# Kernel optimization log

Hardware: AMD Instinct MI355X
Metric: run time of the kernel (lower is better)

The kernel has to match this reference:

```python
import jax, jax.numpy as jnp
import numpy as np

B, DIM, H, W = 8, 128, 64, 64
C, DI, N, R, K = DIM // 4, 2 * (DIM // 4), 16, 2, 4  # chunk dim, d_inner, d_state, dt_rank, n_dirs
L = H * W
EPS = 1e-5


def dwconv(x, w, b, dil):
    # x: [B,C,H,W]; w: [C,1,kh,kw] depthwise; torch padding='same' with dilation
    y = jax.lax.conv_general_dilated(
        x, w, window_strides=(1, 1), padding='SAME', rhs_dilation=(dil, dil),
        dimension_numbers=('NCHW', 'OIHW', 'NCHW'), feature_group_count=x.shape[1])
    return y + b[None, :, None, None]


def layernorm(x, w, b):
    mu = jnp.mean(x, -1, keepdims=True)
    var = jnp.var(x, -1, keepdims=True)
    return (x - mu) * jax.lax.rsqrt(var + EPS) * w + b


def axial_dw(x, mh_w, mh_b, mw_w, mw_b, c_w, c_b, dil):
    skip = x
    x = dwconv(x, mw_w, mw_b, dil)   # (1,7) kernel
    x = dwconv(x, mh_w, mh_b, dil)   # (7,1) kernel
    x = dwconv(x, c_w, c_b, dil)     # 3x3 kernel
    return x + skip


def ss2d(x, in_proj_w, conv_w, conv_b, x_proj_w, dt_proj_w, dt_proj_b,
         A_log, D, out_norm_w, out_norm_b, out_proj_w):
    # x: [B,H,W,C] channels-last (VMamba SS2D)
    b, h, w, _ = x.shape
    xz = jnp.einsum('bhwc,ec->bhwe', x, in_proj_w)          # [B,H,W,2*DI]
    xc, z = jnp.split(xz, 2, axis=-1)
    xc = xc.transpose(0, 3, 1, 2)                           # [B,DI,H,W]
    xc = jax.nn.silu(dwconv(xc, conv_w, conv_b, 1))
    l = h * w
    x_hw = xc.reshape(b, DI, l)
    x_wh = xc.transpose(0, 1, 3, 2).reshape(b, DI, l)
    xs = jnp.stack([x_hw, x_wh], 1)                         # [B,2,DI,L]
    xs = jnp.concatenate([xs, jnp.flip(xs, -1)], 1)         # [B,4,DI,L]
    x_dbl = jnp.einsum('bkdl,kcd->bkcl', xs, x_proj_w)      # c = R+2N
    dts, Bs, Cs = x_dbl[:, :, :R], x_dbl[:, :, R:R + N], x_dbl[:, :, R + N:]
    dts = jnp.einsum('bkrl,kdr->bkdl', dts, dt_proj_w)
    delta = jax.nn.softplus(dts + dt_proj_b[None, :, :, None])  # [B,4,DI,L]
    A = -jnp.exp(A_log)                                     # [4,DI,N]

    def step(hst, inp):
        u_t, dt_t, B_t, C_t = inp  # [B,4,DI],[B,4,DI],[B,4,N],[B,4,N]
        dA = jnp.exp(dt_t[..., None] * A)                   # [B,4,DI,N]
        hst = hst * dA + (dt_t * u_t)[..., None] * B_t[:, :, None, :]
        y = jnp.einsum('bkdn,bkn->bkd', hst, C_t)
        return hst, y

    u_l = jnp.moveaxis(xs, -1, 0)
    dt_l = jnp.moveaxis(delta, -1, 0)
    B_l = jnp.moveaxis(Bs, -1, 0)
    C_l = jnp.moveaxis(Cs, -1, 0)
    h0 = jnp.zeros((b, K, DI, N), xc.dtype)
    _, ys = jax.lax.scan(step, h0, (u_l, dt_l, B_l, C_l))   # [L,B,4,DI]
    out_y = jnp.moveaxis(ys, 0, -1) + D[None, :, :, None] * xs  # [B,4,DI,L]

    inv_y = jnp.flip(out_y[:, 2:4], -1)
    wh_y = out_y[:, 1].reshape(b, DI, w, h).transpose(0, 1, 3, 2).reshape(b, DI, l)
    invwh_y = inv_y[:, 1].reshape(b, DI, w, h).transpose(0, 1, 3, 2).reshape(b, DI, l)
    y = out_y[:, 0] + inv_y[:, 0] + wh_y + invwh_y          # [B,DI,L]
    y = y.transpose(0, 2, 1).reshape(b, h, w, DI)
    y = layernorm(y, out_norm_w, out_norm_b)
    y = y * jax.nn.silu(z)
    return jnp.einsum('bhwd,cd->bhwc', y, out_proj_w)


def setup_inputs() -> dict:
    key = jax.random.key(0)
    ks = iter(jax.random.split(key, 64))
    nrm = lambda s, sc=0.05: jax.random.normal(next(ks), s, jnp.float32) * sc
    inp = {'x': jax.random.normal(next(ks), (B, DIM, H, W), jnp.float32)}
    for i in (1, 2, 3):
        inp[f'dw{i}_mh_w'] = nrm((C, 1, 7, 1), 0.1); inp[f'dw{i}_mh_b'] = nrm((C,), 0.02)
        inp[f'dw{i}_mw_w'] = nrm((C, 1, 1, 7), 0.1); inp[f'dw{i}_mw_b'] = nrm((C,), 0.02)
        inp[f'dw{i}_c_w'] = nrm((C, 1, 3, 3), 0.1); inp[f'dw{i}_c_b'] = nrm((C,), 0.02)
    inp['ln_w'] = jnp.ones((C,)); inp['ln_b'] = jnp.zeros((C,))
    inp['in_proj_w'] = nrm((2 * DI, C))
    inp['conv_w'] = nrm((DI, 1, 3, 3), 0.1); inp['conv_b'] = nrm((DI,), 0.02)
    inp['x_proj_w'] = nrm((K, R + 2 * N, DI))
    inp['dt_proj_w'] = nrm((K, DI, R), 0.1)
    inp['dt_proj_b'] = nrm((K, DI), 0.02)
    inp['A_log'] = jax.random.uniform(next(ks), (K, DI, N), jnp.float32, 0.0, 2.0)
    inp['D'] = jnp.ones((K, DI), jnp.float32)
    inp['out_norm_w'] = jnp.ones((DI,)); inp['out_norm_b'] = jnp.zeros((DI,))
    inp['out_proj_w'] = nrm((C, DI))
    inp['bn_g'] = jnp.ones((DIM,)); inp['bn_b'] = jnp.zeros((DIM,))
    inp['bn_m'] = jnp.zeros((DIM,)); inp['bn_v'] = jnp.ones((DIM,))
    return inp


def reference(x, dw1_mh_w, dw1_mh_b, dw1_mw_w, dw1_mw_b, dw1_c_w, dw1_c_b,
              dw2_mh_w, dw2_mh_b, dw2_mw_w, dw2_mw_b, dw2_c_w, dw2_c_b,
              dw3_mh_w, dw3_mh_b, dw3_mw_w, dw3_mw_b, dw3_c_w, dw3_c_b,
              ln_w, ln_b, in_proj_w, conv_w, conv_b, x_proj_w, dt_proj_w, dt_proj_b,
              A_log, D, out_norm_w, out_norm_b, out_proj_w, bn_g, bn_b, bn_m, bn_v):
    def vss(xc):  # shared VSSBlock: [B,C,H,W] -> [B,C,H,W]
        t = xc.transpose(0, 2, 3, 1)
        t = t + ss2d(layernorm(t, ln_w, ln_b), in_proj_w, conv_w, conv_b, x_proj_w,
                     dt_proj_w, dt_proj_b, A_log, D, out_norm_w, out_norm_b, out_proj_w)
        return t.transpose(0, 3, 1, 2)

    x1, x2, x3, x4 = jnp.split(x, 4, axis=1)
    x1 = vss(axial_dw(x1, dw1_mh_w, dw1_mh_b, dw1_mw_w, dw1_mw_b, dw1_c_w, dw1_c_b, 1))
    x2 = vss(axial_dw(x2, dw2_mh_w, dw2_mh_b, dw2_mw_w, dw2_mw_b, dw2_c_w, dw2_c_b, 2))
    x3 = vss(axial_dw(x3, dw3_mh_w, dw3_mh_b, dw3_mw_w, dw3_mw_b, dw3_c_w, dw3_c_b, 3))
    xc = jnp.concatenate([x1, x2, x3, x4], axis=1)
    # BatchNorm2d in inference mode (running stats)
    y = (xc - bn_m[None, :, None, None]) * jax.lax.rsqrt(bn_v + EPS)[None, :, None, None]
    y = y * bn_g[None, :, None, None] + bn_b[None, :, None, None]
    return jax.nn.relu(y)
```

## Files before the change

### kernel.cpp

```cpp
#include <hip/hip_runtime.h>
#include <math.h>

#define LB __launch_bounds__(256)
#define LB512 __launch_bounds__(512)
#define LB64 __launch_bounds__(64)

#define LOG2E 1.44269504088896340736f
static __device__ __forceinline__ float silu_f(float x){ return x / (1.f + __expf(-x)); }
static __device__ __forceinline__ float softplus_f(float x){
    return (x > 20.f) ? x : __logf(1.f + __expf(x));
}

struct AxialArgs { const float* w[18]; };

__global__ LB void axial_kernel(const float* __restrict__ x, AxialArgs args,
    float* __restrict__ acc,
    const float* __restrict__ bn_g, const float* __restrict__ bn_b,
    const float* __restrict__ bn_m, const float* __restrict__ bn_v,
    float* __restrict__ out)
{
    __shared__ float s0[4096];
    __shared__ float s1[4096];
    if (blockIdx.x >= 768){
        const int gid = (blockIdx.x - 768)*256 + threadIdx.x;
        const int e = gid*4;
        const int l = e & 4095, bc = e >> 12;
        const int c = bc & 31, b = bc >> 5;
        const int ch = 96 + c;
        const size_t idx = ((size_t)b*128+ch)*4096 + l;
        float4 v = *(const float4*)&x[idx];
        const float sc = rsqrtf(bn_v[ch]+1e-5f)*bn_g[ch];
        const float mb = bn_m[ch], bbv = bn_b[ch];
        v.x = fmaxf((v.x-mb)*sc+bbv, 0.f);
        v.y = fmaxf((v.y-mb)*sc+bbv, 0.f);
        v.z = fmaxf((v.z-mb)*sc+bbv, 0.f);
        v.w = fmaxf((v.w-mb)*sc+bbv, 0.f);
        *(float4*)&out[idx] = v;
        return;
    }
    const int chunk = blockIdx.x >> 8;
    const int bc = blockIdx.x & 255;
    const int b = bc >> 5, c = bc & 31;
    const int dil = chunk + 1;
    const float* mh_w = args.w[chunk*6+0];
    const float* mh_b = args.w[chunk*6+1];
    const float* mw_w = args.w[chunk*6+2];
    const float* mw_b = args.w[chunk*6+3];
    const float* cw   = args.w[chunk*6+4];
    const float* cb   = args.w[chunk*6+5];
    const int tid = threadIdx.x;
    const float* xin = x + ((size_t)(b*128 + chunk*32 + c)) * 4096;
    float orig[16];
    #pragma unroll
    for (int kk=0;kk<16;++kk){ float v=xin[tid+kk*256]; orig[kk]=v; s0[tid+kk*256]=v; }
    __syncthreads();

    float w7[7];
    #pragma unroll
    for (int t=0;t<7;++t) w7[t]=mw_w[c*7+t];
    float bias = mw_b[c];
    float v[16];
    #pragma unroll
    for (int kk=0;kk<16;++kk){
        int p=tid+kk*256, i=p>>6, j=p&63;
        float s=bias;
        #pragma unroll
        for (int t=0;t<7;++t){ int jj=j+(t-3)*dil; if (jj>=0&&jj<64) s+=s0[i*64+jj]*w7[t]; }
        v[kk]=s;
    }
    #pragma unroll
    for (int kk=0;kk<16;++kk) s1[tid+kk*256]=v[kk];
    __syncthreads();

    #pragma unroll
    for (int t=0;t<7;++t) w7[t]=mh_w[c*7+t];
    bias = mh_b[c];
    #pragma unroll
    for (int kk=0;kk<16;++kk){
        int p=tid+kk*256, i=p>>6, j=p&63;
        float s=bias;
        #pragma unroll
        for (int t=0;t<7;++t){ int ii=i+(t-3)*dil; if (ii>=0&&ii<64) s+=s1[ii*64+j]*w7[t]; }
        v[kk]=s;
    }
    __syncthreads();
    #pragma unroll
    for (int kk=0;kk<16;++kk) s0[tid+kk*256]=v[kk];
    __syncthreads();

    float w9[9];
    #pragma unroll
    for (int t=0;t<9;++t) w9[t]=cw[c*9+t];
    bias = cb[c];
    float* aout = acc + (size_t)chunk*1048576 + ((size_t)(b*32+c))*4096;
    #pragma unroll
    for (int kk=0;kk<16;++kk){
        int p=tid+kk*256, i=p>>6, j=p&63;
        float s=bias;
        #pragma unroll
        for (int a=0;a<3;++a){
            int ii=i+(a-1)*dil; if (ii<0||ii>=64) continue;
            #pragma unroll
            for (int bb2=0;bb2<3;++bb2){
                int jj=j+(bb2-1)*dil; if (jj<0||jj>=64) continue;
                s += s0[ii*64+jj]*w9[a*3+bb2];
            }
        }
        aout[p] = s + orig[kk];
    }
}

__global__ LB512 void lnproj_kernel(const float* __restrict__ acc, int ch0, size_t cs,
    const float* __restrict__ ln_w, const float* __restrict__ ln_b,
    const float* __restrict__ in_proj_w,
    float* __restrict__ xc, float* __restrict__ z)
{
    __shared__ float s_a[32*65];
    const int cl = blockIdx.x >> 9;
    const int local = blockIdx.x & 511;
    const int chunk = ch0 + cl;
    const int b = local >> 6, lt = local & 63;
    const int l0 = lt*64;
    const int tid = threadIdx.x;
    const float* ab = acc + (size_t)chunk*1048576 + (size_t)b*32*4096 + l0;
    for (int i=tid;i<2048;i+=512){ int c=i>>6, j=i&63; s_a[c*65+j]=ab[(size_t)c*4096 + j]; }
    __syncthreads();
    const int l = tid & 63;
    const int g = __builtin_amdgcn_readfirstlane(tid >> 6);
    float v[32];
    float mu=0.f;
    #pragma unroll
    for (int c=0;c<32;++c){ v[c]=s_a[c*65+l]; mu+=v[c]; }
    mu *= (1.f/32.f);
    float var=0.f;
    #pragma unroll
    for (int c=0;c<32;++c){ float d2=v[c]-mu; var+=d2*d2; }
    var *= (1.f/32.f);
    float rs = rsqrtf(var+1e-5f);
    #pragma unroll
    for (int c=0;c<32;++c) v[c] = (v[c]-mu)*rs*ln_w[c] + ln_b[c];
    float* xcp = xc + (size_t)cl*cs + (size_t)b*64*4096 + l0 + l;
    float* zp  = z  + (size_t)cl*cs + (size_t)b*64*4096 + l0 + l;
    for (int e=g*16; e<g*16+16; ++e){
        const float* wr = in_proj_w + e*32;
        float s=0.f;
        #pragma unroll
        for (int c=0;c<32;++c) s += wr[c]*v[c];
        if (e<64) xcp[(size_t)e*4096]=s; else zp[(size_t)(e-64)*4096]=s;
    }
}

__global__ LB void conv3_kernel(const float* __restrict__ xc, size_t cs,
    const float* __restrict__ conv_w, const float* __restrict__ conv_b,
    float* __restrict__ xconv, float* __restrict__ xconvT)
{
    __shared__ float s0[4096];
    __shared__ float s1[64*65];
    const int cl = blockIdx.x >> 9;
    const int bd = blockIdx.x & 511;
    const int d = bd & 63;
    const int tid = threadIdx.x;
    const float* in = xc + (size_t)cl*cs + (size_t)bd*4096;
    #pragma unroll
    for (int kk=0;kk<16;++kk) s0[tid+kk*256]=in[tid+kk*256];
    __syncthreads();
    float w9[9];
    #pragma unroll
    for (int t=0;t<9;++t) w9[t]=conv_w[d*9+t];
    float bias = conv_b[d];
    float* outp = xconv + (size_t)cl*cs + (size_t)bd*4096;
    #pragma unroll
    for (int kk=0;kk<16;++kk){
        int p=tid+kk*256, i=p>>6, j=p&63;
        float s=bias;
        #pragma unroll
        for (int a=0;a<3;++a){
            int ii=i+a-1; if (ii<0||ii>=64) continue;
            #pragma unroll
            for (int bb2=0;bb2<3;++bb2){
                int jj=j+bb2-1; if (jj<0||jj>=64) continue;
                s += s0[ii*64+jj]*w9[a*3+bb2];
            }
        }
        s = silu_f(s);
        outp[p]=s;
        s1[i*65+j]=s;
    }
    __syncthreads();
    float* outT = xconvT + (size_t)cl*cs + (size_t)bd*4096;
    #pragma unroll
    for (int kk=0;kk<16;++kk){ int p=tid+kk*256; outT[p] = s1[(p&63)*65 + (p>>6)]; }
}

__global__ LB void projscan1_kernel(const float* __restrict__ xconv, const float* __restrict__ xconvT,
    size_t cs,
    const float* __restrict__ x_proj_w, const float* __restrict__ dt_proj_w,
    const float* __restrict__ dt_proj_b, const float* __restrict__ A_log,
    float* __restrict__ Bsb, float* __restrict__ Csb, float* __restrict__ dts_g,
    float* __restrict__ Ssum, float* __restrict__ hloc)
{
    __shared__ float s_x[64*65];
    __shared__ float s_dlt[64*65];
    __shared__ __align__(16) float s_B[1024];
    __shared__ __align__(8) float s_dts[128];
    float* s_Bp = s_dlt;
    float* s_Cp = s_dlt + 1152;
    const int cl = blockIdx.x >> 11;
    const int blkL = blockIdx.x & 2047;
    const int g = blkL & 63, bk = blkL >> 6;
    const int k = bk & 3, b = bk >> 2;
    const int tid = threadIdx.x;
    const int t0 = g*64;
    const float* src = ((k & 1) ? xconvT : xconv) + (size_t)cl*cs;
    const float* sb = src + (size_t)b*64*4096;
    #pragma unroll
    for (int it=0; it<4; ++it){
        const int i4 = tid + it*256;
        const int d = i4 >> 4, jq = (i4 & 15)*4;
        if (k & 2){
            float4 r = *(const float4*)(sb + (size_t)d*4096 + (4092 - t0 - jq));
            s_x[(jq+3)*65 + d] = r.x;
            s_x[(jq+2)*65 + d] = r.y;
            s_x[(jq+1)*65 + d] = r.z;
            s_x[(jq+0)*65 + d] = r.w;
        } else {
            float4 r = *(const float4*)(sb + (size_t)d*4096 + t0 + jq);
            s_x[(jq+0)*65 + d] = r.x;
            s_x[(jq+1)*65 + d] = r.y;
            s_x[(jq+2)*65 + d] = r.z;
            s_x[(jq+3)*65 + d] = r.w;
        }
    }
    __syncthreads();

    {
        const int t = tid & 63;
        const int q = __builtin_amdgcn_readfirstlane(tid >> 6);
        const float* wp = x_proj_w + k*2176;
        float acc9[9];
        #pragma unroll
        for (int r=0;r<9;++r) acc9[r]=0.f;
        const int r0 = q*9;
        const int nr = (q==3)?7:9;
        for (int ch=0; ch<4; ++ch){
            float xv[16];
            #pragma unroll
            for (int i=0;i<16;++i) xv[i] = s_x[t*65 + ch*16 + i];
            #pragma unroll
            for (int r=0;r<9;++r){
                if (r < nr){
                    const float* wr = wp + (r0+r)*64 + ch*16;
                    float s=0.f;
                    #pragma unroll
                    for (int i=0;i<16;++i) s += wr[i]*xv[i];
                    acc9[r] += s;
                }
            }
        }
        #pragma unroll
        for (int r=0;r<9;++r){
            if (r<nr){
                int row = r0 + r;
                if (row < 2)       s_dts[t*2 + row]       = acc9[r];
                else if (row < 18) s_Bp[t*17 + (row-2)]   = acc9[r];
                else               s_Cp[t*17 + (row-18)]  = acc9[r];
            }
        }
    }
    __syncthreads();

    {
        float* BsbC = Bsb + (size_t)cl*cs;
        float* CsbC = Csb + (size_t)cl*cs;
        const size_t tb = (size_t)blkL*1024;
        for (int i=tid;i<1024;i+=256){
            int a = (i>>4)*17 + (i&15);
            float bv = s_Bp[a], cv = s_Cp[a];
            BsbC[tb+i]=bv; CsbC[tb+i]=cv;
            s_B[i]=bv;
        }
        if (tid<128) (dts_g + (size_t)cl*cs)[(size_t)blkL*128 + tid] = s_dts[tid];
    }
    __syncthreads();

    {
        const int d_ = tid & 63, part = tid >> 6;
        const float w0 = dt_proj_w[k*128 + d_*2], w1 = dt_proj_w[k*128 + d_*2 + 1];
        const float bb = dt_proj_b[k*64 + d_];
        #pragma unroll
        for (int i=0;i<16;++i){
            const int t = part*16 + i;
            float dlt = softplus_f(s_dts[t*2]*w0 + s_dts[t*2+1]*w1 + bb);
            s_dlt[t*65 + d_] = dlt;
            s_x[t*65 + d_] *= dlt;
        }
    }
    __syncthreads();

    const int d = tid & 63;
    const int w = __builtin_amdgcn_readfirstlane(tid >> 6);
    float4 Av = *(const float4*)(A_log + ((size_t)(k*64+d)*16 + w*4));
    const float A0 = -__expf(Av.x)*LOG2E, A1 = -__expf(Av.y)*LOG2E,
                A2 = -__expf(Av.z)*LOG2E, A3 = -__expf(Av.w)*LOG2E;
    float h0=0,h1=0,h2=0,h3=0, S=0.f;
    #pragma unroll 4
    for (int t=0;t<64;++t){
        float dlt = s_dlt[t*65+d];
        float du  = s_x[t*65+d];
        S += dlt;
        float4 Bv = *(const float4*)&s_B[t*16 + w*4];
        h0 = h0*exp2f(dlt*A0) + du*Bv.x;
        h1 = h1*exp2f(dlt*A1) + du*Bv.y;
        h2 = h2*exp2f(dlt*A2) + du*Bv.z;
        h3 = h3*exp2f(dlt*A3) + du*Bv.w;
    }
    if (w == 0) (Ssum + (size_t)cl*cs)[(size_t)blkL*64 + d] = S;
    ((float4*)(hloc + (size_t)cl*cs))[(size_t)blkL*256 + d*4 + w] = make_float4(h0,h1,h2,h3);
}

__global__ LB64 void scan2_kernel(const float* __restrict__ Ssum, size_t cs,
    const float* __restrict__ hloc, const float* __restrict__ A_log,
    float* __restrict__ hin)
{
    const int cl = blockIdx.x >> 9;
    const int j = (blockIdx.x & 511)*64 + threadIdx.x;
    const int bk = j >> 10, dn = j & 1023;
    const int k = bk & 3, d = dn >> 4, n = dn & 15;
    const float* SsC = Ssum + (size_t)cl*cs;
    const float* hlC = hloc + (size_t)cl*cs;
    float* hinC = hin + (size_t)cl*cs;
    const float A = -__expf(A_log[(size_t)(k*64+d)*16 + n]) * LOG2E;
    float h = 0.f;
    #pragma unroll 4
    for (int g=0; g<64; ++g){
        const size_t o = ((size_t)bk*64 + g)*1024 + dn;
        hinC[o] = h;
        float S = SsC[((size_t)bk*64 + g)*64 + d];
        h = exp2f(A*S)*h + hlC[o];
    }
}

__global__ LB void scan3_kernel(const float* __restrict__ xconv, const float* __restrict__ xconvT,
    size_t cs,
    const float* __restrict__ Bsb, const float* __restrict__ Csb,
    const float* __restrict__ dts_g,
    const float* __restrict__ dt_proj_w, const float* __restrict__ dt_proj_b,
    const float* __restrict__ A_log, const float* __restrict__ Dp,
    const float* __restrict__ hin, float* __restrict__ outy)
{
    __shared__ __align__(16) float s_B[4][1024];
    __shared__ __align__(16) float s_C[4][1024];
    __shared__ __align__(8) float s_dts[4][128];
    __shared__ float s_y[4][64*17];
    const int cl = blockIdx.x >> 9;
    const int w = threadIdx.x >> 6;
    const int lane = threadIdx.x & 63;
    const int tile = (blockIdx.x & 511)*4 + w;
    const int g = tile & 63, bk = tile >> 6;
    const int k = bk & 3, b = bk >> 2;

    {
        const float4* B4 = (const float4*)(Bsb + (size_t)cl*cs + (size_t)tile*1024);
        const float4* C4 = (const float4*)(Csb + (size_t)cl*cs + (size_t)tile*1024);
        float4* sB4 = (float4*)s_B[w];
        float4* sC4 = (float4*)s_C[w];
        #pragma unroll
        for (int qq=0;qq<4;++qq){ sB4[lane+64*qq]=B4[lane+64*qq]; sC4[lane+64*qq]=C4[lane+64*qq]; }
        const float* dtsC = dts_g + (size_t)cl*cs;
        s_dts[w][lane]      = dtsC[(size_t)tile*128 + lane];
        s_dts[w][lane+64]   = dtsC[(size_t)tile*128 + lane + 64];
    }
    const int d = lane;
    float A[16];
    {
        const float4* Ab = (const float4*)(A_log + (size_t)(k*64+d)*16);
        #pragma unroll
        for (int qq=0;qq<4;++qq){
            float4 v = Ab[qq];
            A[qq*4+0]=-__expf(v.x)*LOG2E; A[qq*4+1]=-__expf(v.y)*LOG2E;
            A[qq*4+2]=-__expf(v.z)*LOG2E; A[qq*4+3]=-__expf(v.w)*LOG2E;
        }
    }
    float h[16];
    {
        const float4* hb = (const float4*)(hin + (size_t)cl*cs + (size_t)tile*1024 + d*16);
        #pragma unroll
        for (int qq=0;qq<4;++qq){
            float4 v=hb[qq];
            h[qq*4+0]=v.x; h[qq*4+1]=v.y; h[qq*4+2]=v.z; h[qq*4+3]=v.w;
        }
    }
    const float w0 = dt_proj_w[k*128 + d*2], w1 = dt_proj_w[k*128 + d*2 + 1];
    const float bb = dt_proj_b[k*64 + d];
    const float Dv = Dp[k*64 + d];
    const float* up = ((k&1)?xconvT:xconv) + (size_t)cl*cs + (size_t)(b*64+d)*4096;
    const float4* sB4 = (const float4*)s_B[w];
    const float4* sC4 = (const float4*)s_C[w];
    float* syw = s_y[w];
    float* obase = outy + (size_t)cl*cs + (size_t)((b*2 + (k&1))*64)*4096;

    for (int t4=0; t4<16; ++t4){
        float u4[4];
        if (k & 2){
            float4 r = *(const float4*)(up + (4092 - g*64 - t4*4));
            u4[0]=r.w; u4[1]=r.z; u4[2]=r.y; u4[3]=r.x;
        } else {
            float4 r = *(const float4*)(up + g*64 + t4*4);
            u4[0]=r.x; u4[1]=r.y; u4[2]=r.z; u4[3]=r.w;
        }
        #pragma unroll
        for (int j=0;j<4;++j){
            const int t = t4*4 + j;
            float2 dtv = *(const float2*)&s_dts[w][t*2];
            float dlt = softplus_f(dtv.x*w0 + dtv.y*w1 + bb);
            float du  = dlt * u4[j];
            float y = 0.f;
            #pragma unroll
            for (int qq=0;qq<4;++qq){
                float4 Bv = sB4[t*4+qq];
                float4 Cv = sC4[t*4+qq];
                h[qq*4+0] = h[qq*4+0]*exp2f(dlt*A[qq*4+0]) + du*Bv.x;
                h[qq*4+1] = h[qq*4+1]*exp2f(dlt*A[qq*4+1]) + du*Bv.y;
                h[qq*4+2] = h[qq*4+2]*exp2f(dlt*A[qq*4+2]) + du*Bv.z;
                h[qq*4+3] = h[qq*4+3]*exp2f(dlt*A[qq*4+3]) + du*Bv.w;
                y += h[qq*4+0]*Cv.x + h[qq*4+1]*Cv.y + h[qq*4+2]*Cv.z + h[qq*4+3]*Cv.w;
            }
            syw[d*17 + (t & 15)] = y + Dv*u4[j];
        }
        if ((t4 & 3) == 3){
            const int tb = t4 >> 2;
            if (k & 2){
                const int colr0 = 4095 - g*64 - tb*16;
                #pragma unroll
                for (int qq=0;qq<16;++qq){
                    int i = qq*64 + lane;
                    int dd = i >> 4, jj = i & 15;
                    atomicAdd(&obase[(size_t)dd*4096 + colr0 - jj], syw[dd*17 + jj]);
                }
            } else {
                const int col0 = g*64 + tb*16;
                #pragma unroll
                for (int qq=0;qq<16;++qq){
                    int i = qq*64 + lane;
                    int dd = i >> 4, jj = i & 15;
                    atomicAdd(&obase[(size_t)dd*4096 + col0 + jj], syw[dd*17 + jj]);
                }
            }
        }
    }
}

__global__ LB void reduce4_kernel(const float* __restrict__ outy, size_t cs,
                                  float* __restrict__ ysum)
{
    __shared__ float s1[64*65];
    const int cl = blockIdx.x >> 9;
    const int local = blockIdx.x & 511;
    const int b = local >> 6, d = local & 63;
    const int tid = threadIdx.x;
    const float* oy = outy + (size_t)cl*cs;
    const float* m0 = oy + ((size_t)((b*2+0)*64 + d))*4096;
    const float* m1 = oy + ((size_t)((b*2+1)*64 + d))*4096;
    #pragma unroll
    for (int it=0; it<16; ++it){
        int p = tid + it*256;
        s1[(p>>6)*65 + (p&63)] = m1[p];
    }
    __syncthreads();
    float* ys = ysum + (size_t)cl*cs + ((size_t)(b*64 + d))*4096;
    #pragma unroll
    for (int it=0; it<16; ++it){
        int p = tid + it*256;
        int i = p >> 6, j = p & 63;
        ys[p] = m0[p] + s1[j*65 + i];
    }
}

__global__ LB512 void combine_kernel(const float* __restrict__ ysum, int ch0, size_t cs,
    const float* __restrict__ z, const float* __restrict__ acc,
    const float* __restrict__ onw, const float* __restrict__ onb,
    const float* __restrict__ opw,
    const float* __restrict__ bn_g, const float* __restrict__ bn_b,
    const float* __restrict__ bn_m, const float* __restrict__ bn_v,
    float* __restrict__ out)
{
    __shared__ float s_red[2][8][64];
    __shared__ float s_y[64*65];
    const int cl = blockIdx.x >> 9;
    const int chunk = ch0 + cl;
    const int local = blockIdx.x & 511;
    const int b = local >> 6, lt = local & 63;
    const int l0 = lt*64;
    const int tid = threadIdx.x;
    const int l = tid & 63;
    const int g = __builtin_amdgcn_readfirstlane(tid >> 6);
    const float* ys = ysum + (size_t)cl*cs + (size_t)b*64*4096;
    const int lf = l0 + l;
    float y[8];
    float psum=0.f, psq=0.f;
    #pragma unroll
    for (int i=0;i<8;++i){
        int d = g*8+i;
        float vv = ys[(size_t)d*4096 + lf];
        y[i]=vv; psum+=vv; psq+=vv*vv;
    }
    s_red[0][g][l]=psum; s_red[1][g][l]=psq;
    __syncthreads();
    float mu=0.f, vsum=0.f;
    #pragma unroll
    for (int gg=0;gg<8;++gg){ mu += s_red[0][gg][l]; vsum += s_red[1][gg][l]; }
    mu *= (1.f/64.f);
    float var = vsum*(1.f/64.f) - mu*mu;
    float rs = rsqrtf(var + 1e-5f);
    const float* zp = z + (size_t)cl*cs + (size_t)b*64*4096 + lf;
    #pragma unroll
    for (int i=0;i<8;++i){
        int d = g*8+i;
        float t2 = (y[i]-mu)*rs*onw[d] + onb[d];
        float zv = zp[(size_t)d*4096];
        s_y[l*65 + d] = t2 * silu_f(zv);
    }
    __syncthreads();
    float a4[4] = {0.f,0.f,0.f,0.f};
    for (int d=0; d<64; ++d){
        float xval = s_y[l*65+d];
        #pragma unroll
        for (int j=0;j<4;++j) a4[j] += opw[(g*4+j)*64+d]*xval;
    }
    const float* ap = acc + (size_t)chunk*1048576 + (size_t)b*32*4096 + lf;
    #pragma unroll
    for (int j=0;j<4;++j){
        int c = g*4+j, ch = chunk*32 + c;
        float s = a4[j] + ap[(size_t)c*4096];
        float bnv = (s - bn_m[ch])*rsqrtf(bn_v[ch]+1e-5f)*bn_g[ch] + bn_b[ch];
        out[((size_t)b*128+ch)*4096 + lf] = fmaxf(bnv, 0.f);
    }
}

extern "C" void kernel_launch(void* const* d_in, const int* in_sizes, int n_in,
                              void* d_out, int out_size, void* d_ws, size_t ws_size,
                              hipStream_t stream) {
    const float* x         = (const float*)d_in[0];
    const float* ln_w      = (const float*)d_in[19];
    const float* ln_b      = (const float*)d_in[20];
    const float* in_proj_w = (const float*)d_in[21];
    const float* conv_w    = (const float*)d_in[22];
    const float* conv_b    = (const float*)d_in[23];
    const float* x_proj_w  = (const float*)d_in[24];
    const float* dt_proj_w = (const float*)d_in[25];
    const float* dt_proj_b = (const float*)d_in[26];
    const float* A_log     = (const float*)d_in[27];
    const float* Dp        = (const float*)d_in[28];
    const float* onw       = (const float*)d_in[29];
    const float* onb       = (const float*)d_in[30];
    const float* opw       = (const float*)d_in[31];
    const float* bn_g      = (const float*)d_in[32];
    const float* bn_b      = (const float*)d_in[33];
    const float* bn_m      = (const float*)d_in[34];
    const float* bn_v      = (const float*)d_in[35];
    float* out = (float*)d_out;

    const size_t F_OUTY = 0;
    const size_t F_XC   = 0;
    const size_t F_HLO  = 2097152;
    const size_t F_Z    = 4194304;
    const size_t F_XCV  = 6291456;
    const size_t F_XCVT = 8388608;
    const size_t F_BSB  = 10485760;
    const size_t F_CSB  = 12582912;
    const size_t F_DTS  = 14680064;
    const size_t F_SSUM = 14942208;
    const size_t F_HIN  = 15073280;
    const size_t CSF    = 17170432;

    float* ws = (float*)d_ws;
    float* acc  = ws;
    float* pool = acc + 3145728;

    const size_t ws_f = ws_size / sizeof(float);
    int nch_max = 1;
    if (ws_f >= 3145728 + 3*CSF) nch_max = 3;
    else if (ws_f >= 3145728 + 2*CSF) nch_max = 2;

    float* xc     = pool + F_XC;
    float* z      = pool + F_Z;
    float* xconv  = pool + F_XCV;
    float* xconvT = pool + F_XCVT;
    float* Bsb    = pool + F_BSB;
    float* Csb    = pool + F_CSB;
    float* dts_g  = pool + F_DTS;
    float* Ssum   = pool + F_SSUM;
    float* hlo    = pool + F_HLO;
    float* hin    = pool + F_HIN;
    float* outy   = pool + F_OUTY;
    float* ysum   = pool + F_XCV;

    AxialArgs aargs;
    for (int chunk=0; chunk<3; ++chunk)
        for (int jj=0; jj<6; ++jj)
            aargs.w[chunk*6+jj] = (const float*)d_in[1 + chunk*6 + jj];
    axial_kernel<<<768+1024, 256, 0, stream>>>(x, aargs, acc, bn_g, bn_b, bn_m, bn_v, out);

    int done = 0;
    while (done < 3){
        const int nch = (3 - done < nch_max) ? (3 - done) : nch_max;
        const size_t cs = (nch > 1) ? CSF : 0;
        const int ch0 = done;

        lnproj_kernel<<<nch*512, 512, 0, stream>>>(acc, ch0, cs, ln_w, ln_b, in_proj_w, xc, z);
        conv3_kernel<<<nch*512, 256, 0, stream>>>(xc, cs, conv_w, conv_b, xconv, xconvT);
        projscan1_kernel<<<nch*2048, 256, 0, stream>>>(xconv, xconvT, cs,
                                                       x_proj_w, dt_proj_w, dt_proj_b,
                                                       A_log, Bsb, Csb, dts_g, Ssum, hlo);
        scan2_kernel<<<nch*512, 64, 0, stream>>>(Ssum, cs, hlo, A_log, hin);
        for (int cl2=0; cl2<nch; ++cl2)
            hipMemsetAsync(outy + (size_t)cl2*cs, 0, (size_t)4194304*sizeof(float), stream);
        scan3_kernel<<<nch*512, 256, 0, stream>>>(xconv, xconvT, cs, Bsb, Csb, dts_g,
                                                  dt_proj_w, dt_proj_b, A_log, Dp, hin, outy);
        reduce4_kernel<<<nch*512, 256, 0, stream>>>(outy, cs, ysum);
        combine_kernel<<<nch*512, 512, 0, stream>>>(ysum, ch0, cs, z, acc, onw, onb, opw,
                                                    bn_g, bn_b, bn_m, bn_v, out);
        done += nch;
    }
}
```

Measured before the change: 424.9 us.

## Split projection and local chunk scan into separate kernels with fp16 delta buffer

Splits the fused projection plus chunk-local scan kernel into a projection kernel and a new scan kernel. The projection kernel now writes softplus deltas to global memory as fp16 and computes per-chunk delta sums. The new scan1b kernel has each thread hold all 16 state values of one channel, where before four waves split the state dimension. scan2 now updates the state buffer in place, which frees the separate hloc buffer. This adds a kernel launch and an extra global round trip for deltas and inputs, and rounding delta to fp16 slightly changes the scan state.

```diff
diff --git a/kernel.cpp b/kernel.cpp
--- a/kernel.cpp
+++ b/kernel.cpp
@@ -1,4 +1,5 @@
 #include <hip/hip_runtime.h>
+#include <hip/hip_fp16.h>
 #include <math.h>
 
 #define LB __launch_bounds__(256)
@@ -192,19 +193,18 @@
     for (int kk=0;kk<16;++kk){ int p=tid+kk*256; outT[p] = s1[(p&63)*65 + (p>>6)]; }
 }
 
-__global__ LB void projscan1_kernel(const float* __restrict__ xconv, const float* __restrict__ xconvT,
+__global__ LB void projgemm_kernel(const float* __restrict__ xconv, const float* __restrict__ xconvT,
     size_t cs,
     const float* __restrict__ x_proj_w, const float* __restrict__ dt_proj_w,
-    const float* __restrict__ dt_proj_b, const float* __restrict__ A_log,
+    const float* __restrict__ dt_proj_b,
     float* __restrict__ Bsb, float* __restrict__ Csb, float* __restrict__ dts_g,
-    float* __restrict__ Ssum, float* __restrict__ hloc)
+    float* __restrict__ Ssum, float* __restrict__ dud_f)
 {
     __shared__ float s_x[64*65];
-    __shared__ float s_dlt[64*65];
-    __shared__ __align__(16) float s_B[1024];
+    __shared__ float s_Bp[64*17];
+    __shared__ float s_Cp[64*17];
     __shared__ __align__(8) float s_dts[128];
-    float* s_Bp = s_dlt;
-    float* s_Cp = s_dlt + 1152;
+    __shared__ float s_Spart[4][64];
     const int cl = blockIdx.x >> 11;
     const int blkL = blockIdx.x & 2047;
     const int g = blkL & 63, bk = blkL >> 6;
@@ -275,68 +275,132 @@
         const size_t tb = (size_t)blkL*1024;
         for (int i=tid;i<1024;i+=256){
             int a = (i>>4)*17 + (i&15);
-            float bv = s_Bp[a], cv = s_Cp[a];
-            BsbC[tb+i]=bv; CsbC[tb+i]=cv;
-            s_B[i]=bv;
+            BsbC[tb+i]=s_Bp[a]; CsbC[tb+i]=s_Cp[a];
         }
         if (tid<128) (dts_g + (size_t)cl*cs)[(size_t)blkL*128 + tid] = s_dts[tid];
     }
-    __syncthreads();
 
     {
         const int d_ = tid & 63, part = tid >> 6;
         const float w0 = dt_proj_w[k*128 + d_*2], w1 = dt_proj_w[k*128 + d_*2 + 1];
         const float bb = dt_proj_b[k*64 + d_];
-        #pragma unroll
-        for (int i=0;i<16;++i){
-            const int t = part*16 + i;
-            float dlt = softplus_f(s_dts[t*2]*w0 + s_dts[t*2+1]*w1 + bb);
-            s_dlt[t*65 + d_] = dlt;
-            s_x[t*65 + d_] *= dlt;
-        }
-    }
-    __syncthreads();
-
-    const int d = tid & 63;
-    const int w = __builtin_amdgcn_readfirstlane(tid >> 6);
-    float4 Av = *(const float4*)(A_log + ((size_t)(k*64+d)*16 + w*4));
-    const float A0 = -__expf(Av.x)*LOG2E, A1 = -__expf(Av.y)*LOG2E,
-                A2 = -__expf(Av.z)*LOG2E, A3 = -__expf(Av.w)*LOG2E;
-    float h0=0,h1=0,h2=0,h3=0, S=0.f;
-    #pragma unroll 4
-    for (int t=0;t<64;++t){
-        float dlt = s_dlt[t*65+d];
-        float du  = s_x[t*65+d];
-        S += dlt;
-        float4 Bv = *(const float4*)&s_B[t*16 + w*4];
-        h0 = h0*exp2f(dlt*A0) + du*Bv.x;
-        h1 = h1*exp2f(dlt*A1) + du*Bv.y;
-        h2 = h2*exp2f(dlt*A2) + du*Bv.z;
-        h3 = h3*exp2f(dlt*A3) + du*Bv.w;
-    }
-    if (w == 0) (Ssum + (size_t)cl*cs)[(size_t)blkL*64 + d] = S;
-    ((float4*)(hloc + (size_t)cl*cs))[(size_t)blkL*256 + d*4 + w] = make_float4(h0,h1,h2,h3);
+        __half* dudC = (__half*)(dud_f + (size_t)cl*cs);
+        float Sp = 0.f;
+        #pragma unroll
+        for (int i4=0;i4<4;++i4){
+            __half hh[4];
+            #pragma unroll
+            for (int j=0;j<4;++j){
+                const int t = part*16 + i4*4 + j;
+                float dlt = softplus_f(s_dts[t*2]*w0 + s_dts[t*2+1]*w1 + bb);
+                hh[j] = __float2half_rn(dlt);
+                Sp += __half2float(hh[j]);
+            }
+            __half2 a = __halves2half2(hh[0], hh[1]);
+            __half2 b2 = __halves2half2(hh[2], hh[3]);
+            uint2 st;
+            st.x = *(unsigned int*)&a;
+            st.y = *(unsigned int*)&b2;
+            *(uint2*)(dudC + (size_t)blkL*4096 + (part*4+i4)*256 + d_*4) = st;
+        }
+        s_Spart[part][d_] = Sp;
+    }
+    __syncthreads();
+    if (tid < 64){
+        (Ssum + (size_t)cl*cs)[(size_t)blkL*64 + tid] =
+            s_Spart[0][tid]+s_Spart[1][tid]+s_Spart[2][tid]+s_Spart[3][tid];
+    }
+}
+
+__global__ LB void scan1b_kernel(const float* __restrict__ xconv, const float* __restrict__ xconvT,
+    size_t cs,
+    const float* __restrict__ Bsb, const float* __restrict__ dud_f,
+    const float* __restrict__ A_log, float* __restrict__ hloc)
+{
+    __shared__ __align__(16) float s_B[4][1024];
+    const int cl = blockIdx.x >> 9;
+    const int w = threadIdx.x >> 6;
+    const int lane = threadIdx.x & 63;
+    const int tile = (blockIdx.x & 511)*4 + w;
+    const int g = tile & 63, bk = tile >> 6;
+    const int k = bk & 3, b = bk >> 2;
+    const int d = lane;
+
+    {
+        const float4* B4 = (const float4*)(Bsb + (size_t)cl*cs + (size_t)tile*1024);
+        float4* sB4 = (float4*)s_B[w];
+        #pragma unroll
+        for (int qq=0;qq<4;++qq) sB4[lane+64*qq]=B4[lane+64*qq];
+    }
+    float A[16];
+    {
+        const float4* Ab = (const float4*)(A_log + (size_t)(k*64+d)*16);
+        #pragma unroll
+        for (int qq=0;qq<4;++qq){
+            float4 v = Ab[qq];
+            A[qq*4+0]=-__expf(v.x)*LOG2E; A[qq*4+1]=-__expf(v.y)*LOG2E;
+            A[qq*4+2]=-__expf(v.z)*LOG2E; A[qq*4+3]=-__expf(v.w)*LOG2E;
+        }
+    }
+    float h[16];
+    #pragma unroll
+    for (int n=0;n<16;++n) h[n]=0.f;
+    const float* up = (((k&1)?xconvT:xconv) + (size_t)cl*cs) + (size_t)(b*64+d)*4096;
+    const __half* dudC = (const __half*)(dud_f + (size_t)cl*cs) + (size_t)tile*4096 + d*4;
+    const float4* sB4 = (const float4*)s_B[w];
+
+    for (int t4=0; t4<16; ++t4){
+        float u4[4];
+        if (k & 2){
+            float4 r = *(const float4*)(up + (4092 - g*64 - t4*4));
+            u4[0]=r.w; u4[1]=r.z; u4[2]=r.y; u4[3]=r.x;
+        } else {
+            float4 r = *(const float4*)(up + g*64 + t4*4);
+            u4[0]=r.x; u4[1]=r.y; u4[2]=r.z; u4[3]=r.w;
+        }
+        uint2 pk = *(const uint2*)(dudC + t4*256);
+        float2 f01 = __half22float2(*(const __half2*)&pk.x);
+        float2 f23 = __half22float2(*(const __half2*)&pk.y);
+        float dl[4] = {f01.x, f01.y, f23.x, f23.y};
+        #pragma unroll
+        for (int j=0;j<4;++j){
+            const int t = t4*4 + j;
+            const float dlt = dl[j];
+            const float du = dlt * u4[j];
+            #pragma unroll
+            for (int qq=0;qq<4;++qq){
+                float4 Bv = sB4[t*4+qq];
+                h[qq*4+0] = h[qq*4+0]*exp2f(dlt*A[qq*4+0]) + du*Bv.x;
+                h[qq*4+1] = h[qq*4+1]*exp2f(dlt*A[qq*4+1]) + du*Bv.y;
+                h[qq*4+2] = h[qq*4+2]*exp2f(dlt*A[qq*4+2]) + du*Bv.z;
+                h[qq*4+3] = h[qq*4+3]*exp2f(dlt*A[qq*4+3]) + du*Bv.w;
+            }
+        }
+    }
+    float4* hb = (float4*)(hloc + (size_t)cl*cs) + (size_t)tile*256 + d*4;
+    #pragma unroll
+    for (int qq=0;qq<4;++qq)
+        hb[qq] = make_float4(h[qq*4+0],h[qq*4+1],h[qq*4+2],h[qq*4+3]);
 }
 
 __global__ LB64 void scan2_kernel(const float* __restrict__ Ssum, size_t cs,
-    const float* __restrict__ hloc, const float* __restrict__ A_log,
-    float* __restrict__ hin)
+    float* __restrict__ hl, const float* __restrict__ A_log)
 {
     const int cl = blockIdx.x >> 9;
     const int j = (blockIdx.x & 511)*64 + threadIdx.x;
     const int bk = j >> 10, dn = j & 1023;
     const int k = bk & 3, d = dn >> 4, n = dn & 15;
     const float* SsC = Ssum + (size_t)cl*cs;
-    const float* hlC = hloc + (size_t)cl*cs;
-    float* hinC = hin + (size_t)cl*cs;
+    float* hlC = hl + (size_t)cl*cs;
     const float A = -__expf(A_log[(size_t)(k*64+d)*16 + n]) * LOG2E;
     float h = 0.f;
     #pragma unroll 4
     for (int g=0; g<64; ++g){
         const size_t o = ((size_t)bk*64 + g)*1024 + dn;
-        hinC[o] = h;
+        float v = hlC[o];
+        hlC[o] = h;
         float S = SsC[((size_t)bk*64 + g)*64 + d];
-        h = exp2f(A*S)*h + hlC[o];
+        h = exp2f(A*S)*h + v;
     }
 }
 
@@ -560,9 +624,9 @@
     const float* bn_v      = (const float*)d_in[35];
     float* out = (float*)d_out;
 
+    const size_t F_DUD  = 0;
+    const size_t F_XC   = 0;
     const size_t F_OUTY = 0;
-    const size_t F_XC   = 0;
-    const size_t F_HLO  = 2097152;
     const size_t F_Z    = 4194304;
     const size_t F_XCV  = 6291456;
     const size_t F_XCVT = 8388608;
@@ -590,9 +654,9 @@
     float* Csb    = pool + F_CSB;
     float* dts_g  = pool + F_DTS;
     float* Ssum   = pool + F_SSUM;
-    float* hlo    = pool + F_HLO;
-    float* hin    = pool + F_HIN;
+    float* hl     = pool + F_HIN;
     float* outy   = pool + F_OUTY;
+    float* dud    = pool + F_DUD;
     float* ysum   = pool + F_XCV;
 
     AxialArgs aargs;
@@ -609,14 +673,15 @@
 
         lnproj_kernel<<<nch*512, 512, 0, stream>>>(acc, ch0, cs, ln_w, ln_b, in_proj_w, xc, z);
         conv3_kernel<<<nch*512, 256, 0, stream>>>(xc, cs, conv_w, conv_b, xconv, xconvT);
-        projscan1_kernel<<<nch*2048, 256, 0, stream>>>(xconv, xconvT, cs,
-                                                       x_proj_w, dt_proj_w, dt_proj_b,
-                                                       A_log, Bsb, Csb, dts_g, Ssum, hlo);
-        scan2_kernel<<<nch*512, 64, 0, stream>>>(Ssum, cs, hlo, A_log, hin);
+        projgemm_kernel<<<nch*2048, 256, 0, stream>>>(xconv, xconvT, cs,
+                                                      x_proj_w, dt_proj_w, dt_proj_b,
+                                                      Bsb, Csb, dts_g, Ssum, dud);
+        scan1b_kernel<<<nch*512, 256, 0, stream>>>(xconv, xconvT, cs, Bsb, dud, A_log, hl);
+        scan2_kernel<<<nch*512, 64, 0, stream>>>(Ssum, cs, hl, A_log);
         for (int cl2=0; cl2<nch; ++cl2)
             hipMemsetAsync(outy + (size_t)cl2*cs, 0, (size_t)4194304*sizeof(float), stream);
         scan3_kernel<<<nch*512, 256, 0, stream>>>(xconv, xconvT, cs, Bsb, Csb, dts_g,
-                                                  dt_proj_w, dt_proj_b, A_log, Dp, hin, outy);
+                                                  dt_proj_w, dt_proj_b, A_log, Dp, hl, outy);
         reduce4_kernel<<<nch*512, 256, 0, stream>>>(outy, cs, ysum);
         combine_kernel<<<nch*512, 512, 0, stream>>>(ysum, ch0, cs, z, acc, onw, onb, opw,
                                                     bn_g, bn_b, bn_m, bn_v, out);
```

Result: slower. 444.7 us (+4.7%).
